# Performance work log

Measured on AMD Instinct MI355X. Metric: run time of the kernel, lower is better.

Reference implementation:

```python
import jax, jax.numpy as jnp
import numpy as np

GROUP_SIZE = 128
INTERMEDIATE = 18944


def _unpack_int4(packed):
    # packed: [rows, cols//8] int32, 8 nibbles per int32 along output dim
    shifts = jnp.arange(8, dtype=jnp.int32) * 4
    nib = (packed[:, :, None] >> shifts) & 15  # [rows, cols//8, 8]
    return nib.reshape(packed.shape[0], packed.shape[1] * 8)


def awq_gemm(x, qweight, qzeros, scales, group_size):
    # Dequantize: W[i,j] = (w4[i,j] - z4[i//g, j]) * scales[i//g, j]
    w = _unpack_int4(qweight).astype(jnp.float32)           # [in, out]
    z = _unpack_int4(qzeros).astype(jnp.float32)            # [in//g, out]
    s = scales.astype(jnp.float32)                          # [in//g, out]
    W = ((w - jnp.repeat(z, group_size, axis=0)) * jnp.repeat(s, group_size, axis=0))
    return (x @ W.astype(x.dtype))                          # [tokens, out]


def setup_inputs() -> dict:
    key = jax.random.key(0)
    ks = jax.random.split(key, 7)
    imax = 2147483647
    return {
        "x": (jax.random.normal(ks[0], (4096, 3584), dtype=jnp.float32) * 0.02).astype(jnp.float16),
        "qweight_gu": jax.random.randint(ks[1], (3584, 4736), 0, imax, dtype=jnp.int32),
        "qzeros_gu": jax.random.randint(ks[2], (28, 4736), 0, imax, dtype=jnp.int32),
        "scales_gu": (jax.random.uniform(ks[3], (28, 37888), dtype=jnp.float32) * 0.01 + 0.001).astype(jnp.float16),
        "qweight_down": jax.random.randint(ks[4], (18944, 448), 0, imax, dtype=jnp.int32),
        "qzeros_down": jax.random.randint(ks[5], (148, 448), 0, imax, dtype=jnp.int32),
        "scales_down": (jax.random.uniform(ks[6], (148, 3584), dtype=jnp.float32) * 0.01 + 0.001).astype(jnp.float16),
    }


def reference(x, qweight_gu, qzeros_gu, scales_gu, qweight_down, qzeros_down, scales_down):
    # Fused gate+up AWQ GEMM (matches forward path after fuse_gate_up())
    gate_up = awq_gemm(x, qweight_gu, qzeros_gu, scales_gu, GROUP_SIZE)  # [T, 2*I]
    gate = gate_up[..., :INTERMEDIATE]
    up = gate_up[..., INTERMEDIATE:]
    intermediate = jax.nn.silu(gate) * up                                # fused SiLU*mul
    down = awq_gemm(intermediate, qweight_down, qzeros_down, scales_down, GROUP_SIZE)
    return down
```

## Files before the change

### kernel.cpp

```cpp
#include <hip/hip_runtime.h>
#include <hip/hip_fp16.h>
#include <stdint.h>

typedef _Float16 half8 __attribute__((ext_vector_type(8)));
typedef _Float16 h2v __attribute__((ext_vector_type(2)));
typedef float f32x16 __attribute__((ext_vector_type(16)));

#define GLD_LDS16(gp, lp)                                                     \
  __builtin_amdgcn_global_load_lds(                                           \
      (const __attribute__((address_space(1))) void*)(gp),                    \
      (__attribute__((address_space(3))) void*)(lp), 16, 0, 0)
#define GLD_LDS4(gp, lp)                                                      \
  __builtin_amdgcn_global_load_lds(                                           \
      (const __attribute__((address_space(1))) void*)(gp),                    \
      (__attribute__((address_space(3))) void*)(lp), 4, 0, 0)

__global__ void xcvt_kernel(const float* __restrict__ in, __half* __restrict__ out) {
  const size_t i = ((size_t)blockIdx.x * 256 + threadIdx.x) * 4;
  float4 v = *(const float4*)(in + i);
  __half2* o = (__half2*)(out + i);
  o[0] = __floats2half2_rn(v.x, v.y);
  o[1] = __floats2half2_rn(v.z, v.w);
}

__global__ void repack_kernel(const int* __restrict__ qw, uint32_t* __restrict__ rp, int P) {
  const int N = P * 8;
  const int n = blockIdx.x * 256 + threadIdx.x;
  const int j8 = n >> 3;
  const int sh = (n & 7) * 4;
  #pragma unroll
  for (int qi = 0; qi < 4; ++qi) {
    const int q = blockIdx.y * 4 + qi;
    const int* src = qw + (size_t)(q * 8) * P + j8;
    uint32_t r = 0;
    #pragma unroll
    for (int t = 0; t < 8; ++t) {
      uint32_t w = ((uint32_t)src[t * P] >> sh) & 15u;
      r |= w << (4 * (t >> 1) + 16 * (t & 1));
    }
    rp[(size_t)q * N + n] = r;
  }
}

__global__ void smz_kernel(const float* __restrict__ sc, const int* __restrict__ qz,
                           uint32_t* __restrict__ smz, int P) {
  const int N = P * 8;
  const int n = blockIdx.x * 256 + threadIdx.x;
  const int g = blockIdx.y;
  uint32_t sbits = __half_as_ushort(__float2half(sc[(size_t)g * N + n]));
  uint32_t z = ((uint32_t)qz[(size_t)g * P + (n >> 3)] >> ((n & 7) * 4)) & 15u;
  uint32_t hz = 0x6400u | z;
  smz[(size_t)g * N + n] = sbits | (hz << 16);
}

union U32H2 { uint32_t u; h2v h; };
__device__ inline h2v bith2(uint32_t u) { U32H2 t; t.u = u; return t.h; }
__device__ inline uint32_t h2bit(h2v h) { U32H2 t; t.h = h; return t.u; }
__device__ inline half8 dequant8(uint32_t p, h2v s, h2v z) {
  union { uint32_t u[4]; half8 v; } r;
  r.u[0] = h2bit((bith2((p & 0x000F000Fu) | 0x64006400u) - z) * s);
  r.u[1] = h2bit((bith2(((p >> 4) & 0x000F000Fu) | 0x64006400u) - z) * s);
  r.u[2] = h2bit((bith2(((p >> 8) & 0x000F000Fu) | 0x64006400u) - z) * s);
  r.u[3] = h2bit((bith2(((p >> 12) & 0x000F000Fu) | 0x64006400u) - z) * s);
  return r.v;
}

template <int KDIM, int NW, int T1OFF, int OW, bool SILU, int NT, int BXS>
__global__ __launch_bounds__(256, 2) void awq_gemm(const __half* __restrict__ A,
                                                   const uint32_t* __restrict__ RP,
                                                   const uint32_t* __restrict__ SMZ,
                                                   void* __restrict__ OUT) {
  constexpr int ABUF = 128 * 64 * 2;
  constexpr int BBUF = NT * 8 * 128 * 4;
  constexpr int BOFF = 3 * ABUF;
  constexpr int ZOFF = BOFF + 3 * BBUF;
  __shared__ __align__(16) unsigned char smem[ZOFF + 2048];

  const int tid = threadIdx.x;
  const int l = tid & 63;
  const int wv = tid >> 6;
  const int l31 = l & 31;
  const int lh = l >> 5;

  const int row0 = blockIdx.y * 128;
  const int n0 = blockIdx.x * BXS;

  const __half* asrc[4];
  #pragma unroll
  for (int it = 0; it < 4; ++it)
    asrc[it] = A + (size_t)(row0 + (tid & 127)) * KDIM + (it * 2 + (tid >> 7)) * 8;

  const uint32_t* bsrc[NT];
  #pragma unroll
  for (int tl = 0; tl < NT; ++tl)
    bsrc[tl] = RP + (size_t)((tid >> 5) & 7) * NW + n0 + tl * T1OFF + (tid & 31) * 4;

  const uint32_t* zsrc = SMZ + n0 + (size_t)(tid >> 7) * T1OFF + (tid & 127);

  f32x16 acc[NT][4];
  #pragma unroll
  for (int tl = 0; tl < NT; ++tl)
    #pragma unroll
    for (int rf = 0; rf < 4; ++rf)
      #pragma unroll
      for (int e = 0; e < 16; ++e) acc[tl][rf][e] = 0.f;

  uint32_t s2[NT], z2[NT];
  constexpr int NSTEP = KDIM / 64;

  const int bbase_l = (wv * 32 + l31) * 4;
  const int arow16 = l31 * 16;

  #pragma unroll
  for (int it = 0; it < 4; ++it)
    GLD_LDS16(asrc[it], &smem[it * 4096 + tid * 16]);
  #pragma unroll
  for (int tl = 0; tl < NT; ++tl)
    GLD_LDS16(bsrc[tl], &smem[BOFF + tl * 4096 + tid * 16]);
  GLD_LDS4(zsrc, &smem[ZOFF + tid * 4]);
  #pragma unroll
  for (int it = 0; it < 4; ++it)
    GLD_LDS16(asrc[it] + 64, &smem[ABUF + it * 4096 + tid * 16]);
  #pragma unroll
  for (int tl = 0; tl < NT; ++tl)
    GLD_LDS16(bsrc[tl] + (size_t)8 * NW, &smem[BOFF + BBUF + tl * 4096 + tid * 16]);

  int cur = 0, stg = 2;
  for (int t = 0; t < NSTEP; ++t) {
    if (t == NSTEP - 1)      asm volatile("s_waitcnt vmcnt(0)" ::: "memory");
    else if (t & 1)          asm volatile("s_waitcnt vmcnt(7)" ::: "memory");
    else                     asm volatile("s_waitcnt vmcnt(6)" ::: "memory");
    __builtin_amdgcn_s_barrier();

    if (t + 2 < NSTEP) {
      #pragma unroll
      for (int it = 0; it < 4; ++it)
        GLD_LDS16(asrc[it] + (size_t)(t + 2) * 64, &smem[stg * ABUF + it * 4096 + tid * 16]);
      #pragma unroll
      for (int tl = 0; tl < NT; ++tl)
        GLD_LDS16(bsrc[tl] + (size_t)(t + 2) * 8 * NW,
                  &smem[BOFF + stg * BBUF + tl * 4096 + tid * 16]);
      if (((t + 2) & 1) == 0) {
        const int g = (t + 2) >> 1;
        GLD_LDS4(zsrc + (size_t)g * NW, &smem[ZOFF + (g & 1) * 1024 + tid * 4]);
      }
    }

    if ((t & 1) == 0) {
      const uint32_t* zl = (const uint32_t*)&smem[ZOFF + ((t >> 1) & 1) * 1024];
      #pragma unroll
      for (int tl = 0; tl < NT; ++tl) {
        uint32_t u = zl[tl * 128 + wv * 32 + l31];
        uint32_t lo = u & 0xFFFFu;
        s2[tl] = lo | (lo << 16);
        z2[tl] = (u & 0xFFFF0000u) | (u >> 16);
      }
    }

    uint32_t bq[NT][4];
    const unsigned char* bbase = &smem[BOFF + cur * BBUF];
    #pragma unroll
    for (int tl = 0; tl < NT; ++tl)
      #pragma unroll
      for (int kf = 0; kf < 4; ++kf)
        bq[tl][kf] = *(const uint32_t*)&bbase[tl * 4096 + (kf * 2 + lh) * 512 + bbase_l];

    const unsigned char* abase = &smem[cur * ABUF];
    #pragma unroll
    for (int kf = 0; kf < 4; ++kf) {
      half8 a[4];
      const int coff = (kf * 2 + lh) * 2048 + arow16;
      #pragma unroll
      for (int rf = 0; rf < 4; ++rf)
        a[rf] = *(const half8*)(abase + coff + rf * 512);
      #pragma unroll
      for (int tl = 0; tl < NT; ++tl) {
        half8 b = dequant8(bq[tl][kf], bith2(s2[tl]), bith2(z2[tl]));
        #pragma unroll
        for (int rf = 0; rf < 4; ++rf)
          acc[tl][rf] =
              __builtin_amdgcn_mfma_f32_32x32x16_f16(a[rf], b, acc[tl][rf], 0, 0, 0);
      }
    }

    cur = (cur == 2) ? 0 : cur + 1;
    stg = (stg == 2) ? 0 : stg + 1;
  }

  if (SILU) {
    __half* O = (__half*)OUT;
    #pragma unroll
    for (int rf = 0; rf < 4; ++rf)
      #pragma unroll
      for (int reg = 0; reg < 16; ++reg) {
        int row = row0 + rf * 32 + (reg & 3) + 8 * (reg >> 2) + 4 * lh;
        int col = n0 + wv * 32 + l31;
        float gf = __half2float(__float2half(acc[0][rf][reg]));
        float uf = __half2float(__float2half(acc[1][rf][reg]));
        float sig = 1.f / (1.f + __expf(-gf));
        float sil = __half2float(__float2half(gf * sig));
        O[(size_t)row * OW + col] = __float2half(sil * uf);
      }
  } else {
    float* O = (float*)OUT;
    #pragma unroll
    for (int tl = 0; tl < NT; ++tl)
      #pragma unroll
      for (int rf = 0; rf < 4; ++rf)
        #pragma unroll
        for (int reg = 0; reg < 16; ++reg) {
          int row = row0 + rf * 32 + (reg & 3) + 8 * (reg >> 2) + 4 * lh;
          int col = n0 + tl * T1OFF + wv * 32 + l31;
          O[(size_t)row * OW + col] = __half2float(__float2half(acc[tl][rf][reg]));
        }
  }
}

extern "C" void kernel_launch(void* const* d_in, const int* in_sizes, int n_in,
                              void* d_out, int out_size, void* d_ws, size_t ws_size,
                              hipStream_t stream) {
  const float* x_f32 = (const float*)d_in[0];
  const int* qw_gu = (const int*)d_in[1];
  const int* qz_gu = (const int*)d_in[2];
  const float* sc_gu = (const float*)d_in[3];
  const int* qw_dn = (const int*)d_in[4];
  const int* qz_dn = (const int*)d_in[5];
  const float* sc_dn = (const float*)d_in[6];

  char* ws = (char*)d_ws;
  __half* interm   = (__half*)ws;
  uint32_t* rp_gu  = (uint32_t*)(ws + 155189248ull);
  uint32_t* smz_gu = (uint32_t*)(ws + 223084544ull);
  __half* xh       = (__half*)(ws + 227328000ull);
  uint32_t* rp_dn  = (uint32_t*)(ws + 155189248ull);
  uint32_t* smz_dn = (uint32_t*)(ws + 189136896ull);

  xcvt_kernel<<<14336, 256, 0, stream>>>(x_f32, xh);
  repack_kernel<<<dim3(148, 112), 256, 0, stream>>>(qw_gu, rp_gu, 4736);
  smz_kernel<<<dim3(148, 28), 256, 0, stream>>>(sc_gu, qz_gu, smz_gu, 4736);

  awq_gemm<3584, 37888, 18944, 18944, true, 2, 128>
      <<<dim3(148, 32), 256, 0, stream>>>(xh, rp_gu, smz_gu, (void*)interm);

  repack_kernel<<<dim3(14, 592), 256, 0, stream>>>(qw_dn, rp_dn, 448);
  smz_kernel<<<dim3(14, 148), 256, 0, stream>>>(sc_dn, qz_dn, smz_dn, 448);

  awq_gemm<18944, 3584, 128, 3584, false, 2, 256>
      <<<dim3(14, 32), 256, 0, stream>>>(interm, rp_dn, smz_dn, d_out);
}
```

Measured before the change: 1.823 ms.

## Shrink GEMM tiles to 128x64 per column-pair with double buffering and higher occupancy

The per-block output tile drops from 128 rows by 256 columns to 128 rows by 128 columns (64 gate plus 64 up). The four waves become a 2x2 split over rows and columns, and the triple-buffered LDS pipeline becomes a double buffer. Scale/zero words are now read straight from global memory into registers instead of being staged in LDS, launch bounds allow 4 blocks per CU, and the grids double. The aim is more blocks and waves to hide latency and better load balance on the small down-projection grid, at the cost of less reuse per tile and more global traffic.

```diff
diff --git a/kernel.cpp b/kernel.cpp
--- a/kernel.cpp
+++ b/kernel.cpp
@@ -10,10 +10,6 @@
   __builtin_amdgcn_global_load_lds(                                           \
       (const __attribute__((address_space(1))) void*)(gp),                    \
       (__attribute__((address_space(3))) void*)(lp), 16, 0, 0)
-#define GLD_LDS4(gp, lp)                                                      \
-  __builtin_amdgcn_global_load_lds(                                           \
-      (const __attribute__((address_space(1))) void*)(gp),                    \
-      (__attribute__((address_space(3))) void*)(lp), 4, 0, 0)
 
 __global__ void xcvt_kernel(const float* __restrict__ in, __half* __restrict__ out) {
   const size_t i = ((size_t)blockIdx.x * 256 + threadIdx.x) * 4;
@@ -65,20 +61,21 @@
   return r.v;
 }
 
-template <int KDIM, int NW, int T1OFF, int OW, bool SILU, int NT, int BXS>
-__global__ __launch_bounds__(256, 2) void awq_gemm(const __half* __restrict__ A,
+template <int KDIM, int NW, int T1OFF, int OW, bool SILU, int BXS>
+__global__ __launch_bounds__(256, 4) void awq_gemm(const __half* __restrict__ A,
                                                    const uint32_t* __restrict__ RP,
                                                    const uint32_t* __restrict__ SMZ,
                                                    void* __restrict__ OUT) {
   constexpr int ABUF = 128 * 64 * 2;
-  constexpr int BBUF = NT * 8 * 128 * 4;
-  constexpr int BOFF = 3 * ABUF;
-  constexpr int ZOFF = BOFF + 3 * BBUF;
-  __shared__ __align__(16) unsigned char smem[ZOFF + 2048];
+  constexpr int BBUF = 8 * 128 * 4;
+  constexpr int BOFF = 2 * ABUF;
+  __shared__ __align__(16) unsigned char smem[2 * ABUF + 2 * BBUF];
 
   const int tid = threadIdx.x;
   const int l = tid & 63;
   const int wv = tid >> 6;
+  const int h = wv >> 1;
+  const int q = wv & 1;
   const int l31 = l & 31;
   const int lh = l >> 5;
 
@@ -90,111 +87,94 @@
   for (int it = 0; it < 4; ++it)
     asrc[it] = A + (size_t)(row0 + (tid & 127)) * KDIM + (it * 2 + (tid >> 7)) * 8;
 
-  const uint32_t* bsrc[NT];
-  #pragma unroll
-  for (int tl = 0; tl < NT; ++tl)
-    bsrc[tl] = RP + (size_t)((tid >> 5) & 7) * NW + n0 + tl * T1OFF + (tid & 31) * 4;
-
-  const uint32_t* zsrc = SMZ + n0 + (size_t)(tid >> 7) * T1OFF + (tid & 127);
-
-  f32x16 acc[NT][4];
-  #pragma unroll
-  for (int tl = 0; tl < NT; ++tl)
-    #pragma unroll
-    for (int rf = 0; rf < 4; ++rf)
-      #pragma unroll
-      for (int e = 0; e < 16; ++e) acc[tl][rf][e] = 0.f;
-
-  uint32_t s2[NT], z2[NT];
+  const int cgrp = (tid & 31) * 4;
+  const uint32_t* bsrc = RP + (size_t)(tid >> 5) * NW +
+                         (cgrp < 64 ? n0 + cgrp : n0 + T1OFF + (cgrp - 64));
+
+  const int scol0 = n0 + q * 32 + l31;
+  const int scol1 = n0 + T1OFF + q * 32 + l31;
+
+  f32x16 acc[2][2];
+  #pragma unroll
+  for (int ct = 0; ct < 2; ++ct)
+    #pragma unroll
+    for (int rf = 0; rf < 2; ++rf)
+      #pragma unroll
+      for (int e = 0; e < 16; ++e) acc[ct][rf][e] = 0.f;
+
   constexpr int NSTEP = KDIM / 64;
-
-  const int bbase_l = (wv * 32 + l31) * 4;
-  const int arow16 = l31 * 16;
+  constexpr int NGRP = KDIM / 128;
+
+  const int arow16 = (h * 64 + l31) * 16;
+  const int bcol0 = (q * 32 + l31) * 4;
 
   #pragma unroll
   for (int it = 0; it < 4; ++it)
     GLD_LDS16(asrc[it], &smem[it * 4096 + tid * 16]);
-  #pragma unroll
-  for (int tl = 0; tl < NT; ++tl)
-    GLD_LDS16(bsrc[tl], &smem[BOFF + tl * 4096 + tid * 16]);
-  GLD_LDS4(zsrc, &smem[ZOFF + tid * 4]);
-  #pragma unroll
-  for (int it = 0; it < 4; ++it)
-    GLD_LDS16(asrc[it] + 64, &smem[ABUF + it * 4096 + tid * 16]);
-  #pragma unroll
-  for (int tl = 0; tl < NT; ++tl)
-    GLD_LDS16(bsrc[tl] + (size_t)8 * NW, &smem[BOFF + BBUF + tl * 4096 + tid * 16]);
-
-  int cur = 0, stg = 2;
+  GLD_LDS16(bsrc, &smem[BOFF + tid * 16]);
+  uint32_t su0 = SMZ[scol0];
+  uint32_t su1 = SMZ[scol1];
+
+  uint32_t s2[2], z2[2];
+
   for (int t = 0; t < NSTEP; ++t) {
-    if (t == NSTEP - 1)      asm volatile("s_waitcnt vmcnt(0)" ::: "memory");
-    else if (t & 1)          asm volatile("s_waitcnt vmcnt(7)" ::: "memory");
-    else                     asm volatile("s_waitcnt vmcnt(6)" ::: "memory");
-    __builtin_amdgcn_s_barrier();
-
-    if (t + 2 < NSTEP) {
+    const int cur = t & 1;
+    __syncthreads();
+
+    if (t + 1 < NSTEP) {
       #pragma unroll
       for (int it = 0; it < 4; ++it)
-        GLD_LDS16(asrc[it] + (size_t)(t + 2) * 64, &smem[stg * ABUF + it * 4096 + tid * 16]);
-      #pragma unroll
-      for (int tl = 0; tl < NT; ++tl)
-        GLD_LDS16(bsrc[tl] + (size_t)(t + 2) * 8 * NW,
-                  &smem[BOFF + stg * BBUF + tl * 4096 + tid * 16]);
-      if (((t + 2) & 1) == 0) {
-        const int g = (t + 2) >> 1;
-        GLD_LDS4(zsrc + (size_t)g * NW, &smem[ZOFF + (g & 1) * 1024 + tid * 4]);
+        GLD_LDS16(asrc[it] + (size_t)(t + 1) * 64,
+                  &smem[(cur ^ 1) * ABUF + it * 4096 + tid * 16]);
+      GLD_LDS16(bsrc + (size_t)(t + 1) * 8 * NW,
+                &smem[BOFF + (cur ^ 1) * BBUF + tid * 16]);
+    }
+
+    if ((t & 1) == 0) {
+      uint32_t lo0 = su0 & 0xFFFFu, lo1 = su1 & 0xFFFFu;
+      s2[0] = lo0 | (lo0 << 16);
+      z2[0] = (su0 & 0xFFFF0000u) | (su0 >> 16);
+      s2[1] = lo1 | (lo1 << 16);
+      z2[1] = (su1 & 0xFFFF0000u) | (su1 >> 16);
+      const int g1 = (t >> 1) + 1;
+      if (g1 < NGRP) {
+        su0 = SMZ[(size_t)g1 * NW + scol0];
+        su1 = SMZ[(size_t)g1 * NW + scol1];
       }
     }
 
-    if ((t & 1) == 0) {
-      const uint32_t* zl = (const uint32_t*)&smem[ZOFF + ((t >> 1) & 1) * 1024];
-      #pragma unroll
-      for (int tl = 0; tl < NT; ++tl) {
-        uint32_t u = zl[tl * 128 + wv * 32 + l31];
-        uint32_t lo = u & 0xFFFFu;
-        s2[tl] = lo | (lo << 16);
-        z2[tl] = (u & 0xFFFF0000u) | (u >> 16);
+    uint32_t bq[2][4];
+    const unsigned char* bbase = &smem[BOFF + cur * BBUF];
+    #pragma unroll
+    for (int ct = 0; ct < 2; ++ct)
+      #pragma unroll
+      for (int kf = 0; kf < 4; ++kf)
+        bq[ct][kf] = *(const uint32_t*)&bbase[(kf * 2 + lh) * 512 + ct * 256 + bcol0];
+
+    const unsigned char* abase = &smem[cur * ABUF];
+    #pragma unroll
+    for (int kf = 0; kf < 4; ++kf) {
+      half8 a[2];
+      const int coff = (kf * 2 + lh) * 2048 + arow16;
+      a[0] = *(const half8*)(abase + coff);
+      a[1] = *(const half8*)(abase + coff + 512);
+      #pragma unroll
+      for (int ct = 0; ct < 2; ++ct) {
+        half8 b = dequant8(bq[ct][kf], bith2(s2[ct]), bith2(z2[ct]));
+        acc[ct][0] = __builtin_amdgcn_mfma_f32_32x32x16_f16(a[0], b, acc[ct][0], 0, 0, 0);
+        acc[ct][1] = __builtin_amdgcn_mfma_f32_32x32x16_f16(a[1], b, acc[ct][1], 0, 0, 0);
       }
     }
-
-    uint32_t bq[NT][4];
-    const unsigned char* bbase = &smem[BOFF + cur * BBUF];
-    #pragma unroll
-    for (int tl = 0; tl < NT; ++tl)
-      #pragma unroll
-      for (int kf = 0; kf < 4; ++kf)
-        bq[tl][kf] = *(const uint32_t*)&bbase[tl * 4096 + (kf * 2 + lh) * 512 + bbase_l];
-
-    const unsigned char* abase = &smem[cur * ABUF];
-    #pragma unroll
-    for (int kf = 0; kf < 4; ++kf) {
-      half8 a[4];
-      const int coff = (kf * 2 + lh) * 2048 + arow16;
-      #pragma unroll
-      for (int rf = 0; rf < 4; ++rf)
-        a[rf] = *(const half8*)(abase + coff + rf * 512);
-      #pragma unroll
-      for (int tl = 0; tl < NT; ++tl) {
-        half8 b = dequant8(bq[tl][kf], bith2(s2[tl]), bith2(z2[tl]));
-        #pragma unroll
-        for (int rf = 0; rf < 4; ++rf)
-          acc[tl][rf] =
-              __builtin_amdgcn_mfma_f32_32x32x16_f16(a[rf], b, acc[tl][rf], 0, 0, 0);
-      }
-    }
-
-    cur = (cur == 2) ? 0 : cur + 1;
-    stg = (stg == 2) ? 0 : stg + 1;
   }
 
   if (SILU) {
     __half* O = (__half*)OUT;
     #pragma unroll
-    for (int rf = 0; rf < 4; ++rf)
+    for (int rf = 0; rf < 2; ++rf)
       #pragma unroll
       for (int reg = 0; reg < 16; ++reg) {
-        int row = row0 + rf * 32 + (reg & 3) + 8 * (reg >> 2) + 4 * lh;
-        int col = n0 + wv * 32 + l31;
+        int row = row0 + h * 64 + rf * 32 + (reg & 3) + 8 * (reg >> 2) + 4 * lh;
+        int col = n0 + q * 32 + l31;
         float gf = __half2float(__float2half(acc[0][rf][reg]));
         float uf = __half2float(__float2half(acc[1][rf][reg]));
         float sig = 1.f / (1.f + __expf(-gf));
@@ -204,14 +184,14 @@
   } else {
     float* O = (float*)OUT;
     #pragma unroll
-    for (int tl = 0; tl < NT; ++tl)
-      #pragma unroll
-      for (int rf = 0; rf < 4; ++rf)
+    for (int ct = 0; ct < 2; ++ct)
+      #pragma unroll
+      for (int rf = 0; rf < 2; ++rf)
         #pragma unroll
         for (int reg = 0; reg < 16; ++reg) {
-          int row = row0 + rf * 32 + (reg & 3) + 8 * (reg >> 2) + 4 * lh;
-          int col = n0 + tl * T1OFF + wv * 32 + l31;
-          O[(size_t)row * OW + col] = __half2float(__float2half(acc[tl][rf][reg]));
+          int row = row0 + h * 64 + rf * 32 + (reg & 3) + 8 * (reg >> 2) + 4 * lh;
+          int col = n0 + ct * T1OFF + q * 32 + l31;
+          O[(size_t)row * OW + col] = __half2float(__float2half(acc[ct][rf][reg]));
         }
   }
 }
@@ -239,12 +219,12 @@
   repack_kernel<<<dim3(148, 112), 256, 0, stream>>>(qw_gu, rp_gu, 4736);
   smz_kernel<<<dim3(148, 28), 256, 0, stream>>>(sc_gu, qz_gu, smz_gu, 4736);
 
-  awq_gemm<3584, 37888, 18944, 18944, true, 2, 128>
-      <<<dim3(148, 32), 256, 0, stream>>>(xh, rp_gu, smz_gu, (void*)interm);
+  awq_gemm<3584, 37888, 18944, 18944, true, 64>
+      <<<dim3(296, 32), 256, 0, stream>>>(xh, rp_gu, smz_gu, (void*)interm);
 
   repack_kernel<<<dim3(14, 592), 256, 0, stream>>>(qw_dn, rp_dn, 448);
   smz_kernel<<<dim3(14, 148), 256, 0, stream>>>(sc_dn, qz_dn, smz_dn, 448);
 
-  awq_gemm<18944, 3584, 128, 3584, false, 2, 256>
-      <<<dim3(14, 32), 256, 0, stream>>>(interm, rp_dn, smz_dn, d_out);
-}
+  awq_gemm<18944, 3584, 64, 3584, false, 128>
+      <<<dim3(28, 32), 256, 0, stream>>>(interm, rp_dn, smz_dn, d_out);
+}
```

After: 2.367 ms. 1.3x slower.
